# Optimization experiments

Hardware: AMD Instinct MI355X
Metric: run time of the kernel (lower is better)

The kernel has to match this reference:

```python
import jax, jax.numpy as jnp
import numpy as np

N_NODES = 100_000
NODES_PER_GRAPH = 100
NUM_GRAPHS = N_NODES // NODES_PER_GRAPH
N_EDGES = 1_600_000
NUM_FEATURES = 32
NUM_CLASSES = 10
K_POOL = 30          # DGCNN sort-pool k
OUT_LEN = 16
IN_LEN = 97          # 32+32+32+1 concatenated GCN features
NUM_ITER = 3


def setup_inputs() -> dict:
    key = jax.random.key(0)
    ks = jax.random.split(key, 12)
    x = jax.random.normal(ks[0], (N_NODES, NUM_FEATURES), dtype=jnp.float32)
    # edges constrained within each graph: gid*npg + local index
    gid = (jnp.arange(N_EDGES) % NUM_GRAPHS).astype(jnp.int64)
    src_loc = jax.random.randint(ks[1], (N_EDGES,), 0, NODES_PER_GRAPH)
    dst_loc = jax.random.randint(ks[2], (N_EDGES,), 0, NODES_PER_GRAPH)
    edge_src = gid * NODES_PER_GRAPH + src_loc
    edge_dst = gid * NODES_PER_GRAPH + dst_loc
    batch = jnp.arange(N_NODES, dtype=jnp.int64) // NODES_PER_GRAPH
    s = 1.0 / np.sqrt(NUM_FEATURES)
    params = dict(
        W1=jax.random.normal(ks[3], (NUM_FEATURES, 32), jnp.float32) * s,
        b1=jnp.zeros((32,), jnp.float32),
        W2=jax.random.normal(ks[4], (32, 32), jnp.float32) * (1/np.sqrt(32)),
        b2=jnp.zeros((32,), jnp.float32),
        W3=jax.random.normal(ks[5], (32, 32), jnp.float32) * (1/np.sqrt(32)),
        b3=jnp.zeros((32,), jnp.float32),
        W4=jax.random.normal(ks[6], (32, 1), jnp.float32) * (1/np.sqrt(32)),
        b4=jnp.zeros((1,), jnp.float32),
        Wcap=jax.random.normal(ks[7], (NUM_CLASSES, OUT_LEN, IN_LEN), jnp.float32) * (1/np.sqrt(IN_LEN)),
    )
    return dict(x=x, edge_src=edge_src, edge_dst=edge_dst, batch=batch, **params)


def gcn_conv(x, W, b, edge_src, edge_dst, dinv):
    # PyG GCNConv: h = xW, out[d] = sum_e dinv[s]*dinv[d]*h[s] (incl. self loops), + b
    h = x @ W
    msg = h[edge_src] * (dinv[edge_src] * dinv[edge_dst])[:, None]
    out = jax.ops.segment_sum(msg, edge_dst, num_segments=x.shape[0])
    out = out + h * (dinv * dinv)[:, None]  # self-loop term
    return out + b


def reference(x, edge_src, edge_dst, batch, W1, b1, W2, b2, W3, b3, W4, b4, Wcap):
    n = x.shape[0]
    # symmetric normalization with self loops (degree over incoming edges + 1)
    deg = jnp.zeros((n,), x.dtype).at[edge_dst].add(1.0) + 1.0
    dinv = jax.lax.rsqrt(deg)

    x1 = jnp.tanh(gcn_conv(x,  W1, b1, edge_src, edge_dst, dinv))
    x2 = jnp.tanh(gcn_conv(x1, W2, b2, edge_src, edge_dst, dinv))
    x3 = jnp.tanh(gcn_conv(x2, W3, b3, edge_src, edge_dst, dinv))
    x4 = jnp.tanh(gcn_conv(x3, W4, b4, edge_src, edge_dst, dinv))
    feat = jnp.concatenate([x1, x2, x3, x4], axis=-1)  # [N, 97]

    # global_sort_pool: per-graph descending sort on last channel, keep top-k nodes
    B = n // NODES_PER_GRAPH
    fg = feat.reshape(B, NODES_PER_GRAPH, IN_LEN)
    order = jnp.argsort(-fg[..., -1], axis=1)[:, :K_POOL]            # [B, k]
    pooled = jnp.take_along_axis(fg, order[..., None], axis=1)        # [B, k, 97]

    # CapsuleLinear, shared weight, k-means routing, Tanimoto similarity
    priors = jnp.einsum('bil,cel->bice', pooled, Wcap)                # [B, k, C, 16]
    pr_sq = jnp.sum(priors * priors, axis=-1)                         # [B, k, C]
    out = jnp.mean(priors, axis=1, keepdims=True)                     # [B, 1, C, 16]
    for _ in range(NUM_ITER):
        xy = jnp.sum(priors * out, axis=-1)                           # [B, k, C]
        out_sq = jnp.sum(out * out, axis=-1)                          # [B, 1, C]
        sim = xy / (pr_sq + out_sq - xy)                              # Tanimoto
        probs = jax.nn.softmax(sim, axis=1)[..., None]                # over in_capsules
        out = jnp.sum(probs * priors, axis=1, keepdims=True)
    out = out[:, 0]                                                   # [B, C, 16]
    classes = jnp.linalg.norm(out, axis=-1)                           # [B, C]
    return classes
```

## Files before the change

kernel.cpp:

```cpp
#include <hip/hip_runtime.h>
#include <math.h>

#define NGRAPH 1000
#define NPG    100
#define EPG    1600
#define NF     32
#define NC     10
#define KP     30
#define OUTL   16
#define INL    97
#define NITER  3

#define NTV    512
#define NTF    1024

#define XSTR   36
#define FSTR   100
#define HSTR   36
#define PSTR   164
#define CSRMAX 1920
#define ZROW   (NPG * XSTR)

#define WS_EDGES_BYTES ((size_t)NGRAPH * EPG * 4)
#define WCAPB_UINT4    2560
#define WS_V10_BYTES   (WS_EDGES_BYTES + (size_t)WCAPB_UINT4 * 16)

#define PIDX(i, c) ((i) * PSTR + (c) * OUTL)

typedef __attribute__((ext_vector_type(8))) short bf16x8;
typedef __attribute__((ext_vector_type(4))) float f32x4;

__device__ __forceinline__ float4 ld4(const float* p) { return *reinterpret_cast<const float4*>(p); }
__device__ __forceinline__ void st4(float* p, float4 v) { *reinterpret_cast<float4*>(p) = v; }
__device__ __forceinline__ float dot4(float4 a, float4 b) { return a.x*b.x + a.y*b.y + a.z*b.z + a.w*b.w; }
__device__ __forceinline__ float tanh_fast(float x) {
  float e = __expf(2.f * x);
  return 1.f - 2.f / (e + 1.f);
}
__device__ __forceinline__ unsigned f2bf(float f) {
  unsigned u = __float_as_uint(f);
  u += 0x7FFFu + ((u >> 16) & 1u);
  return u >> 16;
}

__global__ void prek_edges(const int* __restrict__ esrc, const int* __restrict__ edst,
                           unsigned int* __restrict__ wsE) {
  __shared__ unsigned int t[64][65];
  const int kb = blockIdx.x % (EPG / 64);
  const int gb = blockIdx.x / (EPG / 64);
  const int lane = threadIdx.x & 63;
  const int row  = threadIdx.x >> 6;
  #pragma unroll
  for (int r = row; r < 64; r += 4) {
    int k = kb * 64 + r;
    int g = gb * 64 + lane;
    if (g < NGRAPH) {
      int idx = k * NGRAPH + g;
      int si = esrc[idx] - g * NPG;
      int di = edst[idx] - g * NPG;
      t[r][lane] = (unsigned int)((si << 8) | di);
    }
  }
  __syncthreads();
  #pragma unroll
  for (int r = row; r < 64; r += 4) {
    int g = gb * 64 + r;
    int k = kb * 64 + lane;
    if (g < NGRAPH) wsE[(size_t)g * EPG + k] = t[lane][r];
  }
}

__global__ void prek_capB(const float* __restrict__ Wcap, uint4* __restrict__ wcapB) {
  int o = blockIdx.x * 256 + threadIdx.x;
  if (o >= WCAPB_UINT4) return;
  int ks  = o / 640;
  int rem = o - ks * 640;
  int n   = rem >> 6;
  int ln  = rem & 63;
  int e   = ln & 15;
  int k0  = ks * 32 + ((ln >> 4) << 3);
  const float* wr = Wcap + (n * OUTL + e) * INL;
  unsigned v[8];
  #pragma unroll
  for (int j = 0; j < 8; ++j) {
    int k = k0 + j;
    v[j] = f2bf((k < INL) ? wr[k] : 0.f);
  }
  uint4 pk;
  pk.x = v[0] | (v[1] << 16); pk.y = v[2] | (v[3] << 16);
  pk.z = v[4] | (v[5] << 16); pk.w = v[6] | (v[7] << 16);
  wcapB[o] = pk;
}

struct SMemV10 {
  float feat[NPG * FSTR];
  union {
    struct {
      float hs[(NPG + 1) * XSTR];
      float W[NF * NF];
      float bias2[2][NF];
      unsigned short csr16[CSRMAX];
      int cnt[NPG];
      float dinv[NPG];
      int ptr[NPG + 1];
    } a;
    struct {
      float priors[KP * PSTR];
      float prsq[KP * NC];
      float simbuf[KP * NC];
      float outv[NC * OUTL];
      uint4 pooledB[512];
    } b;
  } u;
  int order[KP];
};

__global__ __launch_bounds__(NTV, 4) void gcn_caps_v10(
    const float* __restrict__ x,
    const unsigned int* __restrict__ wsE,
    const float* __restrict__ W1, const float* __restrict__ b1,
    const float* __restrict__ W2, const float* __restrict__ b2,
    const float* __restrict__ W3, const float* __restrict__ b3,
    const float* __restrict__ W4, const float* __restrict__ b4,
    const uint4* __restrict__ wcapB,
    float* __restrict__ out)
{
  extern __shared__ char smraw[];
  SMemV10& s = *reinterpret_cast<SMemV10*>(smraw);
  const int g = blockIdx.x;
  const int tid = threadIdx.x;

  if (tid < NPG) s.u.a.cnt[tid] = 0;
  if (tid >= 128 && tid < 128 + XSTR) s.u.a.hs[ZROW + (tid - 128)] = 0.f;
  for (int i = tid; i < NF * NF; i += NTV) s.u.a.W[i] = W1[i];
  if (tid < NF) s.u.a.bias2[0][tid] = b1[tid];
  __syncthreads();

  const unsigned int* eg = wsE + (size_t)g * EPG;
  for (int k = tid; k < EPG; k += NTV) atomicAdd(&s.u.a.cnt[eg[k] & 0xFF], 1);
  __syncthreads();

  if (tid < 64) {
    int j = tid;
    int r0 = (2 * j < NPG) ? s.u.a.cnt[2 * j] : 0;
    int r1 = (2 * j + 1 < NPG) ? s.u.a.cnt[2 * j + 1] : 0;
    int p0 = (r0 + 3) & ~3, p1 = (r1 + 3) & ~3;
    int t = p0 + p1;
    int run = t;
    #pragma unroll
    for (int off = 1; off < 64; off <<= 1) {
      int u = __shfl_up(run, off);
      if (j >= off) run += u;
    }
    int excl = run - t;
    if (2 * j < NPG) s.u.a.ptr[2 * j] = excl;
    if (2 * j + 1 < NPG) s.u.a.ptr[2 * j + 1] = excl + p0;
    if (j == 63) s.u.a.ptr[NPG] = run;
  }
  __syncthreads();
  if (tid < NPG) {
    int deg = s.u.a.cnt[tid];
    int p0 = s.u.a.ptr[tid], p1 = s.u.a.ptr[tid + 1];
    s.u.a.dinv[tid] = rsqrtf((float)deg + 1.0f);
    s.u.a.cnt[tid] = p0;
    for (int j = p0 + deg; j < p1; ++j) s.u.a.csr16[j] = (unsigned short)ZROW;
  }
  __syncthreads();

  for (int k = tid; k < EPG; k += NTV) {
    unsigned int p = eg[k];
    int pos = atomicAdd(&s.u.a.cnt[p & 0xFF], 1);
    s.u.a.csr16[pos] = (unsigned short)(((p >> 8) & 0xFF) * XSTR);
  }
  __syncthreads();

  const float4* xr = reinterpret_cast<const float4*>(x + (size_t)g * NPG * NF);

  for (int l = 0; l < 3; ++l) {
    if (tid < 25 * 8) {
      int nd = tid >> 3, cq = tid & 7;
      float4 ac0 = make_float4(0,0,0,0), ac1 = ac0, ac2 = ac0, ac3 = ac0;
      #pragma unroll
      for (int kq = 0; kq < 8; ++kq) {
        float4 a0, a1, a2, a3;
        if (l == 0) {
          a0 = xr[(nd     ) * 8 + kq]; a1 = xr[(nd + 25) * 8 + kq];
          a2 = xr[(nd + 50) * 8 + kq]; a3 = xr[(nd + 75) * 8 + kq];
        } else {
          int cb = (l - 1) * NF + kq * 4;
          a0 = ld4(&s.feat[(nd     ) * FSTR + cb]);
          a1 = ld4(&s.feat[(nd + 25) * FSTR + cb]);
          a2 = ld4(&s.feat[(nd + 50) * FSTR + cb]);
          a3 = ld4(&s.feat[(nd + 75) * FSTR + cb]);
        }
        const float v0[4] = {a0.x, a0.y, a0.z, a0.w};
        const float v1[4] = {a1.x, a1.y, a1.z, a1.w};
        const float v2[4] = {a2.x, a2.y, a2.z, a2.w};
        const float v3[4] = {a3.x, a3.y, a3.z, a3.w};
        #pragma unroll
        for (int j = 0; j < 4; ++j) {
          float4 w4 = ld4(&s.u.a.W[(kq * 4 + j) * NF + cq * 4]);
          ac0.x += v0[j]*w4.x; ac0.y += v0[j]*w4.y; ac0.z += v0[j]*w4.z; ac0.w += v0[j]*w4.w;
          ac1.x += v1[j]*w4.x; ac1.y += v1[j]*w4.y; ac1.z += v1[j]*w4.z; ac1.w += v1[j]*w4.w;
          ac2.x += v2[j]*w4.x; ac2.y += v2[j]*w4.y; ac2.z += v2[j]*w4.z; ac2.w += v2[j]*w4.w;
          ac3.x += v3[j]*w4.x; ac3.y += v3[j]*w4.y; ac3.z += v3[j]*w4.z; ac3.w += v3[j]*w4.w;
        }
      }
      float d0 = s.u.a.dinv[nd], d1 = s.u.a.dinv[nd + 25];
      float d2 = s.u.a.dinv[nd + 50], d3 = s.u.a.dinv[nd + 75];
      ac0.x*=d0; ac0.y*=d0; ac0.z*=d0; ac0.w*=d0;
      ac1.x*=d1; ac1.y*=d1; ac1.z*=d1; ac1.w*=d1;
      ac2.x*=d2; ac2.y*=d2; ac2.z*=d2; ac2.w*=d2;
      ac3.x*=d3; ac3.y*=d3; ac3.z*=d3; ac3.w*=d3;
      st4(&s.u.a.hs[(nd     ) * XSTR + cq * 4], ac0);
      st4(&s.u.a.hs[(nd + 25) * XSTR + cq * 4], ac1);
      st4(&s.u.a.hs[(nd + 50) * XSTR + cq * 4], ac2);
      st4(&s.u.a.hs[(nd + 75) * XSTR + cq * 4], ac3);
    }
    __syncthreads();

    if (l == 0) {
      for (int i = tid; i < NF * NF; i += NTV) s.u.a.W[i] = W2[i];
      if (tid < NF) s.u.a.bias2[1][tid] = b2[tid];
    } else if (l == 1) {
      for (int i = tid; i < NF * NF; i += NTV) s.u.a.W[i] = W3[i];
      if (tid < NF) s.u.a.bias2[0][tid] = b3[tid];
    } else {
      if (tid < NF) s.u.a.W[tid] = W4[tid];
      if (tid == NTV - 1) s.u.a.bias2[1][0] = b4[0];
    }

    for (int o = tid; o < NPG * 16; o += NTV) {
      int d = o >> 4, fq4 = (o & 7) * 4, h = (o >> 3) & 1;
      int p0 = s.u.a.ptr[d], p1 = s.u.a.ptr[d + 1];
      float4 r = (h == 0) ? ld4(&s.u.a.hs[d * XSTR + fq4])
                          : make_float4(0.f, 0.f, 0.f, 0.f);
      for (int idx = p0 + h * 4; idx < p1; idx += 8) {
        uint2 c2 = *reinterpret_cast<const uint2*>(&s.u.a.csr16[idx]);
        int o0 = c2.x & 0xFFFF, o1 = c2.x >> 16;
        int o2 = c2.y & 0xFFFF, o3 = c2.y >> 16;
        float4 h0 = ld4(&s.u.a.hs[o0 + fq4]);
        float4 h1 = ld4(&s.u.a.hs[o1 + fq4]);
        float4 h2 = ld4(&s.u.a.hs[o2 + fq4]);
        float4 h3 = ld4(&s.u.a.hs[o3 + fq4]);
        r.x += (h0.x + h1.x) + (h2.x + h3.x);
        r.y += (h0.y + h1.y) + (h2.y + h3.y);
        r.z += (h0.z + h1.z) + (h2.z + h3.z);
        r.w += (h0.w + h1.w) + (h2.w + h3.w);
      }
      r.x += __shfl_xor(r.x, 8);
      r.y += __shfl_xor(r.y, 8);
      r.z += __shfl_xor(r.z, 8);
      r.w += __shfl_xor(r.w, 8);
      if (h == 0) {
        const float* bc = s.u.a.bias2[l & 1];
        float4 bq = ld4(&bc[fq4]);
        float di = s.u.a.dinv[d];
        float4 oo;
        oo.x = tanh_fast(di * r.x + bq.x);
        oo.y = tanh_fast(di * r.y + bq.y);
        oo.z = tanh_fast(di * r.z + bq.z);
        oo.w = tanh_fast(di * r.w + bq.w);
        st4(&s.feat[d * FSTR + l * NF + fq4], oo);
      }
    }
    __syncthreads();
  }

  if (tid < NPG) {
    float a = 0.f;
    #pragma unroll
    for (int kq = 0; kq < 8; ++kq)
      a += dot4(ld4(&s.feat[tid * FSTR + 2 * NF + kq * 4]), ld4(&s.u.a.W[kq * 4]));
    s.u.a.hs[tid * XSTR] = a * s.u.a.dinv[tid];
  }
  __syncthreads();
  for (int o = tid; o < NPG * 8; o += NTV) {
    int d = o >> 3, p = o & 7;
    int p0 = s.u.a.ptr[d], p1 = s.u.a.ptr[d + 1];
    float r = (p == 0) ? s.u.a.hs[d * XSTR] : 0.f;
    for (int idx = p0 + p; idx < p1; idx += 8) r += s.u.a.hs[s.u.a.csr16[idx]];
    r += __shfl_xor(r, 1);
    r += __shfl_xor(r, 2);
    r += __shfl_xor(r, 4);
    if (p == 0)
      s.feat[d * FSTR + 96] = tanh_fast(s.u.a.dinv[d] * r + s.u.a.bias2[1][0]);
  }
  __syncthreads();

  if (tid < NPG * 4) {
    int i = tid >> 2, p = tid & 3;
    float vv = s.feat[i * FSTR + 96];
    int j0 = p * 25, j1 = j0 + 25;
    int rank = 0;
    for (int j = j0; j < j1; ++j) {
      float vj = s.feat[j * FSTR + 96];
      rank += (vj > vv) || (vj == vv && j < i);
    }
    rank += __shfl_xor(rank, 1);
    rank += __shfl_xor(rank, 2);
    if (p == 0 && rank < KP) s.order[rank] = i;
  }
  __syncthreads();

  {
    int mt = tid >> 8, ks = (tid >> 6) & 3, ln = tid & 63;
    int i = mt * 16 + (ln & 15);
    int k0 = ks * 32 + ((ln >> 4) << 3);
    uint4 pk = make_uint4(0, 0, 0, 0);
    if (i < KP) {
      int row = s.order[i] * FSTR;
      float f[8];
      if (ks < 3) {
        float4 x0 = ld4(&s.feat[row + k0]);
        float4 x1 = ld4(&s.feat[row + k0 + 4]);
        f[0]=x0.x; f[1]=x0.y; f[2]=x0.z; f[3]=x0.w;
        f[4]=x1.x; f[5]=x1.y; f[6]=x1.z; f[7]=x1.w;
      } else {
        #pragma unroll
        for (int j = 0; j < 8; ++j) f[j] = 0.f;
        if (k0 == 96) f[0] = s.feat[row + 96];
      }
      pk.x = f2bf(f[0]) | (f2bf(f[1]) << 16);
      pk.y = f2bf(f[2]) | (f2bf(f[3]) << 16);
      pk.z = f2bf(f[4]) | (f2bf(f[5]) << 16);
      pk.w = f2bf(f[6]) | (f2bf(f[7]) << 16);
    }
    s.u.b.pooledB[(mt * 4 + ks) * 64 + ln] = pk;
  }
  __syncthreads();

  if (tid < 5 * 64) {
    int w = tid >> 6, ln = tid & 63;
    #pragma unroll
    for (int mt = 0; mt < 2; ++mt) {
      bf16x8 afr[4];
      #pragma unroll
      for (int ks = 0; ks < 4; ++ks) {
        uint4 raw = s.u.b.pooledB[(mt * 4 + ks) * 64 + ln];
        afr[ks] = __builtin_bit_cast(bf16x8, raw);
      }
      #pragma unroll
      for (int nn = 0; nn < 2; ++nn) {
        int n = w * 2 + nn;
        f32x4 acc = {0.f, 0.f, 0.f, 0.f};
        #pragma unroll
        for (int ks = 0; ks < 4; ++ks) {
          uint4 braw = wcapB[(ks * 10 + n) * 64 + ln];
          bf16x8 bfr = __builtin_bit_cast(bf16x8, braw);
          acc = __builtin_amdgcn_mfma_f32_16x16x32_bf16(afr[ks], bfr, acc, 0, 0, 0);
        }
        int ibase = mt * 16 + ((ln >> 4) << 2);
        int e = ln & 15;
        #pragma unroll
        for (int j = 0; j < 4; ++j) {
          int i = ibase + j;
          if (i < KP) s.u.b.priors[PIDX(i, n) + e] = acc[j];
        }
      }
    }
  }
  __syncthreads();

  if (tid < KP * NC) {
    int i = tid / NC, c = tid % NC;
    const float* pr = &s.u.b.priors[PIDX(i, c)];
    float a = 0.f;
    #pragma unroll
    for (int eq = 0; eq < 4; ++eq) { float4 p = ld4(pr + eq * 4); a += dot4(p, p); }
    s.u.b.prsq[tid] = a;
  }
  if (tid < NC * OUTL) {
    int c = tid >> 4, e = tid & 15;
    float a = 0.f;
    #pragma unroll
    for (int i = 0; i < KP; ++i) a += s.u.b.priors[PIDX(i, c) + e];
    s.u.b.outv[tid] = a * (1.0f / KP);
  }
  __syncthreads();

  for (int it = 0; it < NITER; ++it) {
    if (tid < KP * NC) {
      int i = tid / NC, c = tid % NC;
      const float* pr = &s.u.b.priors[PIDX(i, c)];
      const float* ov = &s.u.b.outv[c * OUTL];
      float xy = 0.f, oq = 0.f;
      #pragma unroll
      for (int eq = 0; eq < 4; ++eq) {
        float4 p = ld4(pr + eq * 4);
        float4 o = ld4(ov + eq * 4);
        xy += dot4(p, o); oq += dot4(o, o);
      }
      s.u.b.simbuf[tid] = xy / (s.u.b.prsq[tid] + oq - xy);
    }
    __syncthreads();
    if (tid < NC * OUTL) {
      int c = tid >> 4, e = tid & 15;
      float m = -1e30f;
      #pragma unroll
      for (int i = 0; i < KP; ++i) m = fmaxf(m, s.u.b.simbuf[i * NC + c]);
      float ss = 0.f, a = 0.f;
      #pragma unroll
      for (int i = 0; i < KP; ++i) {
        float w = __expf(s.u.b.simbuf[i * NC + c] - m);
        ss += w;
        a += w * s.u.b.priors[PIDX(i, c) + e];
      }
      s.u.b.outv[tid] = a / ss;
    }
    __syncthreads();
  }

  if (tid < NC) {
    const float* ov = &s.u.b.outv[tid * OUTL];
    float a = 0.f;
    #pragma unroll
    for (int eq = 0; eq < 4; ++eq) { float4 o = ld4(ov + eq * 4); a += dot4(o, o); }
    out[(size_t)g * NC + tid] = sqrtf(a);
  }
}

struct SMemF {
  float feat[NPG * FSTR];
  union {
    unsigned short epack[EPG];
    float priors[KP * PSTR];
  } u;
  union {
    float hs[NPG * HSTR];
    struct {
      float prsq[KP * NC];
      float simbuf[KP * NC];
      float outv[NC * OUTL];
      float smax[NC];
      float ssum[NC];
      int   order[KP];
    } r;
  } v;
  float W[NF * NF];
  float bias2[2][NF];
  unsigned char csr[EPG];
  int ptr[NPG + 1];
  int cnt[NPG];
  float dinv[NPG];
};

__global__ __launch_bounds__(NTF, 8) void gcn_caps_fused(
    const float* __restrict__ x,
    const int* __restrict__ esrc, const int* __restrict__ edst,
    const float* __restrict__ W1, const float* __restrict__ b1,
    const float* __restrict__ W2, const float* __restrict__ b2,
    const float* __restrict__ W3, const float* __restrict__ b3,
    const float* __restrict__ W4, const float* __restrict__ b4,
    const float* __restrict__ Wcap,
    float* __restrict__ out)
{
  extern __shared__ char smem_raw[];
  SMemF& s = *reinterpret_cast<SMemF*>(smem_raw);
  const int g = blockIdx.x;
  const int tid = threadIdx.x;

  if (tid < NPG) s.cnt[tid] = 0;
  for (int i = tid; i < NF * NF; i += NTF) s.W[i] = W1[i];
  if (tid < NF) s.bias2[0][tid] = b1[tid];
  __syncthreads();

  for (int k = tid; k < EPG; k += NTF) {
    int si = esrc[g + k * NGRAPH] - g * NPG;
    int di = edst[g + k * NGRAPH] - g * NPG;
    s.u.epack[k] = (unsigned short)((si << 8) | di);
    atomicAdd(&s.cnt[di], 1);
  }
  __syncthreads();

  if (tid < 64) {
    int j = tid;
    int a0 = (2 * j < NPG) ? s.cnt[2 * j] : 0;
    int a1 = (2 * j + 1 < NPG) ? s.cnt[2 * j + 1] : 0;
    int t = a0 + a1;
    int run = t;
    #pragma unroll
    for (int off = 1; off < 64; off <<= 1) {
      int u = __shfl_up(run, off);
      if (j >= off) run += u;
    }
    int excl = run - t;
    if (2 * j < NPG) s.ptr[2 * j] = excl;
    if (2 * j + 1 < NPG) s.ptr[2 * j + 1] = excl + a0;
    if (j == 63) s.ptr[NPG] = run;
  }
  __syncthreads();
  if (tid < NPG) {
    s.dinv[tid] = rsqrtf((float)s.cnt[tid] + 1.0f);
    s.cnt[tid] = s.ptr[tid];
  }
  __syncthreads();

  for (int k = tid; k < EPG; k += NTF) {
    int pk = s.u.epack[k];
    int pos = atomicAdd(&s.cnt[pk & 0xFF], 1);
    s.csr[pos] = (unsigned char)(pk >> 8);
  }
  __syncthreads();

  const float4* xr = reinterpret_cast<const float4*>(x + (size_t)g * NPG * NF);
  for (int l = 0; l < 3; ++l) {
    if (tid < NPG * 8) {
      int node = tid >> 3, cq = tid & 7;
      float4 acc = make_float4(0.f, 0.f, 0.f, 0.f);
      #pragma unroll
      for (int kq = 0; kq < 8; ++kq) {
        float4 a4 = (l == 0) ? xr[node * 8 + kq]
                             : ld4(&s.feat[node * FSTR + (l - 1) * NF + kq * 4]);
        const float av[4] = {a4.x, a4.y, a4.z, a4.w};
        #pragma unroll
        for (int j = 0; j < 4; ++j) {
          float4 w4 = ld4(&s.W[(kq * 4 + j) * NF + cq * 4]);
          acc.x += av[j] * w4.x; acc.y += av[j] * w4.y;
          acc.z += av[j] * w4.z; acc.w += av[j] * w4.w;
        }
      }
      float di = s.dinv[node];
      acc.x *= di; acc.y *= di; acc.z *= di; acc.w *= di;
      st4(&s.v.hs[node * HSTR + ((cq ^ (node >> 3)) & 7) * 4], acc);
    }
    __syncthreads();

    if (l == 0) {
      for (int i = tid; i < NF * NF; i += NTF) s.W[i] = W2[i];
      if (tid < NF) s.bias2[1][tid] = b2[tid];
    } else if (l == 1) {
      for (int i = tid; i < NF * NF; i += NTF) s.W[i] = W3[i];
      if (tid < NF) s.bias2[0][tid] = b3[tid];
    } else {
      if (tid < NF) s.W[tid] = W4[tid];
      if (tid == NTF - 1) s.bias2[1][0] = b4[0];
    }

    if (tid < NPG * 8) {
      int d = tid >> 3, fq = tid & 7;
      const float* bc = s.bias2[l & 1];
      float4 b4q = ld4(&bc[fq * 4]);
      float4 r = ld4(&s.v.hs[d * HSTR + ((fq ^ (d >> 3)) & 7) * 4]);
      int p0 = s.ptr[d], p1 = s.ptr[d + 1];
      int idx = p0;
      for (; idx + 1 < p1; idx += 2) {
        int sc0 = s.csr[idx], sc1 = s.csr[idx + 1];
        float4 h0 = ld4(&s.v.hs[sc0 * HSTR + ((fq ^ (sc0 >> 3)) & 7) * 4]);
        float4 h1 = ld4(&s.v.hs[sc1 * HSTR + ((fq ^ (sc1 >> 3)) & 7) * 4]);
        r.x += h0.x + h1.x; r.y += h0.y + h1.y;
        r.z += h0.z + h1.z; r.w += h0.w + h1.w;
      }
      if (idx < p1) {
        int sc = s.csr[idx];
        float4 hq = ld4(&s.v.hs[sc * HSTR + ((fq ^ (sc >> 3)) & 7) * 4]);
        r.x += hq.x; r.y += hq.y; r.z += hq.z; r.w += hq.w;
      }
      float di = s.dinv[d];
      float4 o;
      o.x = tanh_fast(di * r.x + b4q.x);
      o.y = tanh_fast(di * r.y + b4q.y);
      o.z = tanh_fast(di * r.z + b4q.z);
      o.w = tanh_fast(di * r.w + b4q.w);
      st4(&s.feat[d * FSTR + l * NF + fq * 4], o);
    }
    __syncthreads();
  }

  float* hsf = s.v.hs;
  if (tid < NPG) {
    float a = 0.f;
    #pragma unroll
    for (int kq = 0; kq < 8; ++kq)
      a += dot4(ld4(&s.feat[tid * FSTR + 64 + kq * 4]), ld4(&s.W[kq * 4]));
    hsf[tid] = a * s.dinv[tid];
  }
  __syncthreads();
  if (tid < NPG) {
    float r = hsf[tid];
    int p0 = s.ptr[tid], p1 = s.ptr[tid + 1];
    for (int idx = p0; idx < p1; ++idx) r += hsf[s.csr[idx]];
    s.feat[tid * FSTR + 96] = tanh_fast(s.dinv[tid] * r + s.bias2[1][0]);
  }
  __syncthreads();

  if (tid < NPG * 8) {
    int i = tid >> 3, p = tid & 7;
    float vv = s.feat[i * FSTR + 96];
    int j0 = p * 13, j1 = min(NPG, j0 + 13);
    int rank = 0;
    for (int j = j0; j < j1; ++j) {
      float vj = s.feat[j * FSTR + 96];
      rank += (vj > vv) || (vj == vv && j < i);
    }
    rank += __shfl_xor(rank, 1);
    rank += __shfl_xor(rank, 2);
    rank += __shfl_xor(rank, 4);
    if (p == 0 && rank < KP) s.v.r.order[rank] = i;
  }
  __syncthreads();

  if (tid < KP * OUTL) {
    int i = tid >> 4, e = tid & 15;
    int row = s.v.r.order[i] * FSTR;
    float acc[NC];
    #pragma unroll
    for (int c = 0; c < NC; ++c) acc[c] = 0.f;
    for (int c = 0; c < NC; ++c) {
      float a = 0.f;
      for (int l = 0; l < INL; ++l) a += s.feat[row + l] * Wcap[(c * OUTL + e) * INL + l];
      acc[c] = a;
    }
    #pragma unroll
    for (int c = 0; c < NC; ++c) s.u.priors[PIDX(i, c) + e] = acc[c];
  }
  __syncthreads();

  if (tid < KP * NC) {
    int i = tid / NC, c = tid % NC;
    const float* pr = &s.u.priors[PIDX(i, c)];
    float a = 0.f;
    #pragma unroll
    for (int eq = 0; eq < 4; ++eq) { float4 p = ld4(pr + eq * 4); a += dot4(p, p); }
    s.v.r.prsq[tid] = a;
  }
  if (tid < NC * OUTL) {
    int c = tid >> 4, e = tid & 15;
    float a = 0.f;
    #pragma unroll
    for (int i = 0; i < KP; ++i) a += s.u.priors[PIDX(i, c) + e];
    s.v.r.outv[tid] = a * (1.0f / KP);
  }
  __syncthreads();

  for (int it = 0; it < NITER; ++it) {
    if (tid < KP * NC) {
      int i = tid / NC, c = tid % NC;
      const float* pr = &s.u.priors[PIDX(i, c)];
      const float* ov = &s.v.r.outv[c * OUTL];
      float xy = 0.f, oq = 0.f;
      #pragma unroll
      for (int eq = 0; eq < 4; ++eq) {
        float4 p = ld4(pr + eq * 4);
        float4 o = ld4(ov + eq * 4);
        xy += dot4(p, o); oq += dot4(o, o);
      }
      s.v.r.simbuf[tid] = xy / (s.v.r.prsq[tid] + oq - xy);
    }
    __syncthreads();
    if (tid < NC) {
      float m = -1e30f;
      #pragma unroll
      for (int i = 0; i < KP; ++i) m = fmaxf(m, s.v.r.simbuf[i * NC + tid]);
      float ss = 0.f;
      #pragma unroll
      for (int i = 0; i < KP; ++i) ss += __expf(s.v.r.simbuf[i * NC + tid] - m);
      s.v.r.smax[tid] = m;
      s.v.r.ssum[tid] = 1.f / ss;
    }
    __syncthreads();
    if (tid < NC * OUTL) {
      int c = tid >> 4, e = tid & 15;
      float m = s.v.r.smax[c], is = s.v.r.ssum[c], a = 0.f;
      #pragma unroll
      for (int i = 0; i < KP; ++i)
        a += __expf(s.v.r.simbuf[i * NC + c] - m) * s.u.priors[PIDX(i, c) + e];
      s.v.r.outv[tid] = a * is;
    }
    __syncthreads();
  }

  if (tid < NC) {
    const float* ov = &s.v.r.outv[tid * OUTL];
    float a = 0.f;
    #pragma unroll
    for (int eq = 0; eq < 4; ++eq) { float4 o = ld4(ov + eq * 4); a += dot4(o, o); }
    out[(size_t)g * NC + tid] = sqrtf(a);
  }
}

extern "C" void kernel_launch(void* const* d_in, const int* in_sizes, int n_in,
                              void* d_out, int out_size, void* d_ws, size_t ws_size,
                              hipStream_t stream) {
  const float* x    = (const float*)d_in[0];
  const int*   esrc = (const int*)d_in[1];
  const int*   edst = (const int*)d_in[2];
  const float* W1 = (const float*)d_in[4];
  const float* b1 = (const float*)d_in[5];
  const float* W2 = (const float*)d_in[6];
  const float* b2 = (const float*)d_in[7];
  const float* W3 = (const float*)d_in[8];
  const float* b3 = (const float*)d_in[9];
  const float* W4 = (const float*)d_in[10];
  const float* b4 = (const float*)d_in[11];
  const float* Wcap = (const float*)d_in[12];
  float* outp = (float*)d_out;

  if (ws_size >= WS_V10_BYTES) {
    unsigned int* wsE = (unsigned int*)d_ws;
    uint4* wcapB = (uint4*)((char*)d_ws + WS_EDGES_BYTES);
    (void)hipFuncSetAttribute((const void*)gcn_caps_v10,
                              hipFuncAttributeMaxDynamicSharedMemorySize, (int)sizeof(SMemV10));
    prek_edges<<<(EPG / 64) * 16, 256, 0, stream>>>(esrc, edst, wsE);
    prek_capB<<<(WCAPB_UINT4 + 255) / 256, 256, 0, stream>>>(Wcap, wcapB);
    gcn_caps_v10<<<NGRAPH, NTV, sizeof(SMemV10), stream>>>(
        x, wsE, W1, b1, W2, b2, W3, b3, W4, b4, wcapB, outp);
  } else {
    (void)hipFuncSetAttribute((const void*)gcn_caps_fused,
                              hipFuncAttributeMaxDynamicSharedMemorySize, (int)sizeof(SMemF));
    gcn_caps_fused<<<NGRAPH, NTF, sizeof(SMemF), stream>>>(
        x, esrc, edst, W1, b1, W2, b2, W3, b3, W4, b4, Wcap, outp);
  }
}
```

Before: 82.05 us.

## Keep capsule routing in MFMA registers with wave shuffles instead of shared memory

The capsule stage now keeps MFMA accumulator outputs in registers. Each wave runs the prior-norm, mean, Tanimoto similarity, softmax routing and final norm for its two classes using cross-lane shuffles, which removes the shared-memory priors/prsq/simbuf/outv buffers and the block-wide barriers between routing steps. The CSR setup folds the dinv and padding work into the scan step to drop one barrier. The W4 projection is spread over 8 lanes per node with a shuffle reduction, and W4/b4 are preloaded during layer 1 into dedicated slots. The cost is more registers per thread and many shuffle reductions, and shared memory use shrinks, which may help occupancy.

```diff
diff --git a/kernel.cpp b/kernel.cpp
--- a/kernel.cpp
+++ b/kernel.cpp
@@ -92,30 +92,28 @@
   wcapB[o] = pk;
 }
 
-struct SMemV10 {
+struct SMemV11 {
   float feat[NPG * FSTR];
   union {
     struct {
       float hs[(NPG + 1) * XSTR];
       float W[NF * NF];
+      float W4s[NF];
       float bias2[2][NF];
+      float b4s;
       unsigned short csr16[CSRMAX];
       int cnt[NPG];
       float dinv[NPG];
       int ptr[NPG + 1];
     } a;
     struct {
-      float priors[KP * PSTR];
-      float prsq[KP * NC];
-      float simbuf[KP * NC];
-      float outv[NC * OUTL];
       uint4 pooledB[512];
     } b;
   } u;
   int order[KP];
 };
 
-__global__ __launch_bounds__(NTV, 4) void gcn_caps_v10(
+__global__ __launch_bounds__(NTV, 4) void gcn_caps_v12(
     const float* __restrict__ x,
     const unsigned int* __restrict__ wsE,
     const float* __restrict__ W1, const float* __restrict__ b1,
@@ -126,7 +124,7 @@
     float* __restrict__ out)
 {
   extern __shared__ char smraw[];
-  SMemV10& s = *reinterpret_cast<SMemV10*>(smraw);
+  SMemV11& s = *reinterpret_cast<SMemV11*>(smraw);
   const int g = blockIdx.x;
   const int tid = threadIdx.x;
 
@@ -142,10 +140,11 @@
 
   if (tid < 64) {
     int j = tid;
-    int r0 = (2 * j < NPG) ? s.u.a.cnt[2 * j] : 0;
-    int r1 = (2 * j + 1 < NPG) ? s.u.a.cnt[2 * j + 1] : 0;
-    int p0 = (r0 + 3) & ~3, p1 = (r1 + 3) & ~3;
-    int t = p0 + p1;
+    int n0 = 2 * j, n1 = 2 * j + 1;
+    int r0 = (n0 < NPG) ? s.u.a.cnt[n0] : 0;
+    int r1 = (n1 < NPG) ? s.u.a.cnt[n1] : 0;
+    int q0 = (r0 + 3) & ~3, q1 = (r1 + 3) & ~3;
+    int t = q0 + q1;
     int run = t;
     #pragma unroll
     for (int off = 1; off < 64; off <<= 1) {
@@ -153,17 +152,20 @@
       if (j >= off) run += u;
     }
     int excl = run - t;
-    if (2 * j < NPG) s.u.a.ptr[2 * j] = excl;
-    if (2 * j + 1 < NPG) s.u.a.ptr[2 * j + 1] = excl + p0;
+    if (n0 < NPG) {
+      s.u.a.ptr[n0] = excl;
+      s.u.a.dinv[n0] = rsqrtf((float)r0 + 1.0f);
+      s.u.a.cnt[n0] = excl;
+      for (int k = excl + r0; k < excl + q0; ++k) s.u.a.csr16[k] = (unsigned short)ZROW;
+    }
+    if (n1 < NPG) {
+      int e1 = excl + q0;
+      s.u.a.ptr[n1] = e1;
+      s.u.a.dinv[n1] = rsqrtf((float)r1 + 1.0f);
+      s.u.a.cnt[n1] = e1;
+      for (int k = e1 + r1; k < e1 + q1; ++k) s.u.a.csr16[k] = (unsigned short)ZROW;
+    }
     if (j == 63) s.u.a.ptr[NPG] = run;
-  }
-  __syncthreads();
-  if (tid < NPG) {
-    int deg = s.u.a.cnt[tid];
-    int p0 = s.u.a.ptr[tid], p1 = s.u.a.ptr[tid + 1];
-    s.u.a.dinv[tid] = rsqrtf((float)deg + 1.0f);
-    s.u.a.cnt[tid] = p0;
-    for (int j = p0 + deg; j < p1; ++j) s.u.a.csr16[j] = (unsigned short)ZROW;
   }
   __syncthreads();
 
@@ -225,9 +227,8 @@
     } else if (l == 1) {
       for (int i = tid; i < NF * NF; i += NTV) s.u.a.W[i] = W3[i];
       if (tid < NF) s.u.a.bias2[0][tid] = b3[tid];
-    } else {
-      if (tid < NF) s.u.a.W[tid] = W4[tid];
-      if (tid == NTV - 1) s.u.a.bias2[1][0] = b4[0];
+      if (tid >= 64 && tid < 64 + NF) s.u.a.W4s[tid - 64] = W4[tid - 64];
+      if (tid == NTV - 1) s.u.a.b4s = b4[0];
     }
 
     for (int o = tid; o < NPG * 16; o += NTV) {
@@ -267,14 +268,16 @@
     __syncthreads();
   }
 
-  if (tid < NPG) {
-    float a = 0.f;
-    #pragma unroll
-    for (int kq = 0; kq < 8; ++kq)
-      a += dot4(ld4(&s.feat[tid * FSTR + 2 * NF + kq * 4]), ld4(&s.u.a.W[kq * 4]));
-    s.u.a.hs[tid * XSTR] = a * s.u.a.dinv[tid];
-  }
-  __syncthreads();
+  for (int o = tid; o < NPG * 8; o += NTV) {
+    int d = o >> 3, fq4 = (o & 7) * 4;
+    float r = dot4(ld4(&s.feat[d * FSTR + 2 * NF + fq4]), ld4(&s.u.a.W4s[fq4]));
+    r += __shfl_xor(r, 1);
+    r += __shfl_xor(r, 2);
+    r += __shfl_xor(r, 4);
+    if ((o & 7) == 0) s.u.a.hs[d * XSTR] = r * s.u.a.dinv[d];
+  }
+  __syncthreads();
+
   for (int o = tid; o < NPG * 8; o += NTV) {
     int d = o >> 3, p = o & 7;
     int p0 = s.u.a.ptr[d], p1 = s.u.a.ptr[d + 1];
@@ -284,7 +287,7 @@
     r += __shfl_xor(r, 2);
     r += __shfl_xor(r, 4);
     if (p == 0)
-      s.feat[d * FSTR + 96] = tanh_fast(s.u.a.dinv[d] * r + s.u.a.bias2[1][0]);
+      s.feat[d * FSTR + 96] = tanh_fast(s.u.a.dinv[d] * r + s.u.a.b4s);
   }
   __syncthreads();
 
@@ -332,91 +335,76 @@
 
   if (tid < 5 * 64) {
     int w = tid >> 6, ln = tid & 63;
-    #pragma unroll
-    for (int mt = 0; mt < 2; ++mt) {
-      bf16x8 afr[4];
+    int q = ln >> 4;
+    bf16x8 afr[2][4];
+    #pragma unroll
+    for (int mt = 0; mt < 2; ++mt)
+      #pragma unroll
+      for (int ks = 0; ks < 4; ++ks)
+        afr[mt][ks] = __builtin_bit_cast(bf16x8, s.u.b.pooledB[(mt * 4 + ks) * 64 + ln]);
+    #pragma unroll
+    for (int nn = 0; nn < 2; ++nn) {
+      int n = w * 2 + nn;
+      f32x4 acc0 = {0.f, 0.f, 0.f, 0.f}, acc1 = {0.f, 0.f, 0.f, 0.f};
       #pragma unroll
       for (int ks = 0; ks < 4; ++ks) {
-        uint4 raw = s.u.b.pooledB[(mt * 4 + ks) * 64 + ln];
-        afr[ks] = __builtin_bit_cast(bf16x8, raw);
-      }
-      #pragma unroll
-      for (int nn = 0; nn < 2; ++nn) {
-        int n = w * 2 + nn;
-        f32x4 acc = {0.f, 0.f, 0.f, 0.f};
+        bf16x8 bfr = __builtin_bit_cast(bf16x8, wcapB[(ks * 10 + n) * 64 + ln]);
+        acc0 = __builtin_amdgcn_mfma_f32_16x16x32_bf16(afr[0][ks], bfr, acc0, 0, 0, 0);
+        acc1 = __builtin_amdgcn_mfma_f32_16x16x32_bf16(afr[1][ks], bfr, acc1, 0, 0, 0);
+      }
+      float p[8];
+      #pragma unroll
+      for (int j = 0; j < 4; ++j) { p[j] = acc0[j]; p[4 + j] = acc1[j]; }
+      float prsq[8];
+      #pragma unroll
+      for (int sl = 0; sl < 8; ++sl) {
+        float t = p[sl] * p[sl];
+        t += __shfl_xor(t, 1); t += __shfl_xor(t, 2);
+        t += __shfl_xor(t, 4); t += __shfl_xor(t, 8);
+        prsq[sl] = t;
+      }
+      float outv = 0.f;
+      #pragma unroll
+      for (int sl = 0; sl < 8; ++sl) outv += p[sl];
+      outv += __shfl_xor(outv, 16); outv += __shfl_xor(outv, 32);
+      outv *= (1.0f / KP);
+      #pragma unroll
+      for (int it = 0; it < NITER; ++it) {
+        float oq = outv * outv;
+        oq += __shfl_xor(oq, 1); oq += __shfl_xor(oq, 2);
+        oq += __shfl_xor(oq, 4); oq += __shfl_xor(oq, 8);
+        float sim[8];
         #pragma unroll
-        for (int ks = 0; ks < 4; ++ks) {
-          uint4 braw = wcapB[(ks * 10 + n) * 64 + ln];
-          bf16x8 bfr = __builtin_bit_cast(bf16x8, braw);
-          acc = __builtin_amdgcn_mfma_f32_16x16x32_bf16(afr[ks], bfr, acc, 0, 0, 0);
+        for (int sl = 0; sl < 8; ++sl) {
+          float t = p[sl] * outv;
+          t += __shfl_xor(t, 1); t += __shfl_xor(t, 2);
+          t += __shfl_xor(t, 4); t += __shfl_xor(t, 8);
+          sim[sl] = t / (prsq[sl] + oq - t);
         }
-        int ibase = mt * 16 + ((ln >> 4) << 2);
-        int e = ln & 15;
+        float m = -1e30f;
         #pragma unroll
-        for (int j = 0; j < 4; ++j) {
-          int i = ibase + j;
-          if (i < KP) s.u.b.priors[PIDX(i, n) + e] = acc[j];
+        for (int sl = 0; sl < 8; ++sl) {
+          int i = ((sl >> 2) << 4) + (q << 2) + (sl & 3);
+          if (i < KP) m = fmaxf(m, sim[sl]);
         }
-      }
-    }
-  }
-  __syncthreads();
-
-  if (tid < KP * NC) {
-    int i = tid / NC, c = tid % NC;
-    const float* pr = &s.u.b.priors[PIDX(i, c)];
-    float a = 0.f;
-    #pragma unroll
-    for (int eq = 0; eq < 4; ++eq) { float4 p = ld4(pr + eq * 4); a += dot4(p, p); }
-    s.u.b.prsq[tid] = a;
-  }
-  if (tid < NC * OUTL) {
-    int c = tid >> 4, e = tid & 15;
-    float a = 0.f;
-    #pragma unroll
-    for (int i = 0; i < KP; ++i) a += s.u.b.priors[PIDX(i, c) + e];
-    s.u.b.outv[tid] = a * (1.0f / KP);
-  }
-  __syncthreads();
-
-  for (int it = 0; it < NITER; ++it) {
-    if (tid < KP * NC) {
-      int i = tid / NC, c = tid % NC;
-      const float* pr = &s.u.b.priors[PIDX(i, c)];
-      const float* ov = &s.u.b.outv[c * OUTL];
-      float xy = 0.f, oq = 0.f;
-      #pragma unroll
-      for (int eq = 0; eq < 4; ++eq) {
-        float4 p = ld4(pr + eq * 4);
-        float4 o = ld4(ov + eq * 4);
-        xy += dot4(p, o); oq += dot4(o, o);
-      }
-      s.u.b.simbuf[tid] = xy / (s.u.b.prsq[tid] + oq - xy);
-    }
-    __syncthreads();
-    if (tid < NC * OUTL) {
-      int c = tid >> 4, e = tid & 15;
-      float m = -1e30f;
-      #pragma unroll
-      for (int i = 0; i < KP; ++i) m = fmaxf(m, s.u.b.simbuf[i * NC + c]);
-      float ss = 0.f, a = 0.f;
-      #pragma unroll
-      for (int i = 0; i < KP; ++i) {
-        float w = __expf(s.u.b.simbuf[i * NC + c] - m);
-        ss += w;
-        a += w * s.u.b.priors[PIDX(i, c) + e];
-      }
-      s.u.b.outv[tid] = a / ss;
-    }
-    __syncthreads();
-  }
-
-  if (tid < NC) {
-    const float* ov = &s.u.b.outv[tid * OUTL];
-    float a = 0.f;
-    #pragma unroll
-    for (int eq = 0; eq < 4; ++eq) { float4 o = ld4(ov + eq * 4); a += dot4(o, o); }
-    out[(size_t)g * NC + tid] = sqrtf(a);
+        m = fmaxf(m, __shfl_xor(m, 16)); m = fmaxf(m, __shfl_xor(m, 32));
+        float ssum = 0.f, onew = 0.f;
+        #pragma unroll
+        for (int sl = 0; sl < 8; ++sl) {
+          int i = ((sl >> 2) << 4) + (q << 2) + (sl & 3);
+          float wg = (i < KP) ? __expf(sim[sl] - m) : 0.f;
+          ssum += wg;
+          onew += wg * p[sl];
+        }
+        ssum += __shfl_xor(ssum, 16); ssum += __shfl_xor(ssum, 32);
+        onew += __shfl_xor(onew, 16); onew += __shfl_xor(onew, 32);
+        outv = onew / ssum;
+      }
+      float t = outv * outv;
+      t += __shfl_xor(t, 1); t += __shfl_xor(t, 2);
+      t += __shfl_xor(t, 4); t += __shfl_xor(t, 8);
+      if (ln == 0) out[(size_t)g * NC + n] = sqrtf(t);
+    }
   }
 }
 
@@ -699,11 +687,11 @@
   if (ws_size >= WS_V10_BYTES) {
     unsigned int* wsE = (unsigned int*)d_ws;
     uint4* wcapB = (uint4*)((char*)d_ws + WS_EDGES_BYTES);
-    (void)hipFuncSetAttribute((const void*)gcn_caps_v10,
-                              hipFuncAttributeMaxDynamicSharedMemorySize, (int)sizeof(SMemV10));
+    (void)hipFuncSetAttribute((const void*)gcn_caps_v12,
+                              hipFuncAttributeMaxDynamicSharedMemorySize, (int)sizeof(SMemV11));
     prek_edges<<<(EPG / 64) * 16, 256, 0, stream>>>(esrc, edst, wsE);
     prek_capB<<<(WCAPB_UINT4 + 255) / 256, 256, 0, stream>>>(Wcap, wcapB);
-    gcn_caps_v10<<<NGRAPH, NTV, sizeof(SMemV10), stream>>>(
+    gcn_caps_v12<<<NGRAPH, NTV, sizeof(SMemV11), stream>>>(
         x, wsE, W1, b1, W2, b2, W3, b3, W4, b4, wcapB, outp);
   } else {
     (void)hipFuncSetAttribute((const void*)gcn_caps_fused,
```

New measurement: 107.2 us. +30.6%, slower.
